# Kernel tuning notes

Hardware: AMD Instinct MI355X
Metric: run time of the kernel (lower is better)

The kernel has to match this reference:

```python
import jax, jax.numpy as jnp
import numpy as np
import math

B, SQ, SK, D = 32, 2048, 2048, 128


def setup_inputs() -> dict:
    key = jax.random.key(0)
    kq, kk, kv = jax.random.split(key, 3)
    queries = jax.random.normal(kq, (B, SQ, D), dtype=jnp.float32)
    keys = jax.random.normal(kk, (B, SK, D), dtype=jnp.float32)
    values = jax.random.normal(kv, (B, SK, D), dtype=jnp.float32)
    # causal mask: True = masked (future positions), broadcast over batch
    causal = jnp.triu(jnp.ones((SQ, SK), dtype=bool), k=1)
    mask = jnp.broadcast_to(causal, (B, SQ, SK))
    return {"queries": queries, "keys": keys, "values": values, "mask": mask}


def reference(queries, keys, values, mask):
    d = queries.shape[-1]
    scale = 1.0 / math.sqrt(d)
    # [B, Sq, Sk] score matrix (the module materializes this explicitly)
    scores = jnp.einsum("bqd,bkd->bqk", queries, keys) * scale
    scores = jnp.where(mask, -jnp.inf, scores)
    attn = jax.nn.softmax(scores, axis=-1)
    # dropout p=0.0 -> identity (eval parity)
    return jnp.einsum("bqk,bkd->bqd", attn, values)
```

## Files before the change

### kernel.cpp

```cpp
#include <hip/hip_runtime.h>
#include <hip/hip_bf16.h>

#define NB   32
#define SQL  2048
#define DH   128
#define QBLK 128
#define KBLK 64
#define NKT  (SQL / KBLK)
#define TILEB 16384

typedef __attribute__((ext_vector_type(4)))  float f32x4;
typedef __attribute__((ext_vector_type(16))) float f32x16;
typedef __attribute__((ext_vector_type(8)))  short s16x8;
typedef __attribute__((ext_vector_type(4)))  unsigned int u32x4;

__device__ __forceinline__ unsigned int cvtpk_bf16(float lo, float hi) {
  unsigned int r;
  asm("v_cvt_pk_bf16_f32 %0, %1, %2" : "=v"(r) : "v"(lo), "v"(hi));
  return r;
}
#define PLSWAP(x, y) asm volatile("v_permlane32_swap_b32 %0, %1" : "+v"(x), "+v"(y))

__device__ __forceinline__ unsigned int pk2(float lo, float hi) {
  unsigned short a = __builtin_bit_cast(unsigned short, __float2bfloat16(lo));
  unsigned short b = __builtin_bit_cast(unsigned short, __float2bfloat16(hi));
  return (unsigned int)a | ((unsigned int)b << 16);
}

#define AS1(p) ((const __attribute__((address_space(1))) void*)(p))
#define AS3(p) ((__attribute__((address_space(3))) void*)(p))

__global__ __launch_bounds__(256)
void prep_kv(const float* __restrict__ Kg, const float* __restrict__ Vg,
             char* __restrict__ wsK, char* __restrict__ wsV) {
  const int blk = blockIdx.x;
  const int b   = blk >> 5;
  const int kt  = blk & 31;
  const int tid = threadIdx.x;
  const float* Ksrc = Kg + ((size_t)b * SQL + (size_t)kt * KBLK) * DH;
  const float* Vsrc = Vg + ((size_t)b * SQL + (size_t)kt * KBLK) * DH;
  char* Kdst = wsK + (size_t)blk * TILEB;
  char* Vdst = wsV + (size_t)blk * TILEB;

  {
    const int q16 = tid & 15;
    const int r0  = tid >> 4;
    #pragma unroll
    for (int it = 0; it < 4; ++it) {
      const int r = r0 + 16 * it;
      const float* src = Ksrc + (size_t)r * DH + 8 * q16;
      f32x4 a = *(const f32x4*)(src);
      f32x4 d = *(const f32x4*)(src + 4);
      u32x4 w;
      w[0] = pk2(a[0], a[1]); w[1] = pk2(a[2], a[3]);
      w[2] = pk2(d[0], d[1]); w[3] = pk2(d[2], d[3]);
      *(u32x4*)(Kdst + ((r * 256 + 16 * q16) ^ ((r & 7) << 4))) = w;
    }
  }
  {
    const int kq = tid & 15;
    const int dq = tid >> 4;
    #pragma unroll
    for (int it = 0; it < 2; ++it) {
      const int d0 = 4 * dq + 64 * it;
      f32x4 rv[4];
      #pragma unroll
      for (int j = 0; j < 4; ++j)
        rv[j] = *(const f32x4*)(Vsrc + (size_t)(4 * kq + j) * DH + d0);
      #pragma unroll
      for (int j2 = 0; j2 < 4; ++j2) {
        const int dd = d0 + j2;
        uint2 w = make_uint2(pk2(rv[0][j2], rv[1][j2]), pk2(rv[2][j2], rv[3][j2]));
        *(uint2*)(Vdst + ((dd * 128 + 8 * kq) ^ ((dd & 7) << 4))) = w;
      }
    }
  }
}

__global__ __launch_bounds__(256, 2)
void attn_fwd(const float* __restrict__ Qg, const char* __restrict__ wsK,
              const char* __restrict__ wsV, float* __restrict__ Og) {
  __shared__ __align__(16) char smem[65536];

  const int tid  = threadIdx.x;
  const int wid  = tid >> 6;
  const int lane = tid & 63;
  const int hi   = lane >> 5;
  const int c    = lane & 31;

  const int i    = blockIdx.x;
  const int half = i >> 8;
  const int j    = i & 255;
  const int b    = j & 31;
  const int q3   = j >> 5;
  const int qt   = half ? (15 - q3) : q3;
  const int qb   = qt * QBLK;
  const int nt   = 2 * qt + 2;

  const float* Qb = Qg + (size_t)b * SQL * DH;
  float* Ob = Og + (size_t)b * SQL * DH;
  const char* Ktiles = wsK + (size_t)b * NKT * TILEB;
  const char* Vtiles = wsV + (size_t)b * NKT * TILEB;

  const float qscale = 0.08838834764831845f * 1.4426950408889634f;

  s16x8 qf[8];
  {
    const float* qr = Qb + (size_t)(qb + 32*wid + c) * DH + 8*hi;
    #pragma unroll
    for (int ds = 0; ds < 8; ++ds) {
      f32x4 a = *(const f32x4*)(qr + 16*ds);
      f32x4 d = *(const f32x4*)(qr + 16*ds + 4);
      u32x4 w;
      w[0] = pk2(a[0]*qscale, a[1]*qscale);
      w[1] = pk2(a[2]*qscale, a[3]*qscale);
      w[2] = pk2(d[0]*qscale, d[1]*qscale);
      w[3] = pk2(d[2]*qscale, d[3]*qscale);
      qf[ds] = __builtin_bit_cast(s16x8, w);
    }
  }

  f32x16 oacc[4];
  #pragma unroll
  for (int nb = 0; nb < 4; ++nb) oacc[nb] = (f32x16){0.f};
  float m_run = -1e30f, l_run = 0.f;

  const int qglob = qb + 32*wid + c;
  const int qhiw  = qb + 32*wid + 31;
  const int qlow  = qb + 32*wid;

  auto STAGE = [&](int t) {
    const char* ks = Ktiles + (size_t)t * TILEB + tid * 16;
    const char* vs = Vtiles + (size_t)t * TILEB + tid * 16;
    char* kl = smem + (t & 1) * 16384 + wid * 1024;
    char* vl = smem + 32768 + (t & 1) * 16384 + wid * 1024;
    #pragma unroll
    for (int jj = 0; jj < 4; ++jj) {
      __builtin_amdgcn_global_load_lds(AS1(ks + jj * 4096), AS3(kl + jj * 4096), 16, 0, 0);
      __builtin_amdgcn_global_load_lds(AS1(vs + jj * 4096), AS3(vl + jj * 4096), 16, 0, 0);
    }
  };

  STAGE(0);

  for (int t = 0; t < nt; ++t) {
    asm volatile("s_waitcnt vmcnt(0)" ::: "memory");
    __builtin_amdgcn_s_barrier();
    __builtin_amdgcn_sched_barrier(0);
    if (t + 1 < nt) STAGE(t + 1);

    const int kb = t * KBLK;
    const char* Kl = smem + (t & 1) * 16384;
    const char* Vl = smem + 32768 + (t & 1) * 16384;

    if (kb <= qhiw) {
      f32x16 sacc[2];
      sacc[0] = (f32x16){0.f};
      sacc[1] = (f32x16){0.f};
      __builtin_amdgcn_s_setprio(1);
      #pragma unroll
      for (int ds = 0; ds < 8; ++ds) {
        #pragma unroll
        for (int mb = 0; mb < 2; ++mb) {
          const int row = 32*mb + c;
          s16x8 kf = *(const s16x8*)(Kl + ((row*256 + 32*ds + 16*hi) ^ ((c & 7) << 4)));
          sacc[mb] = __builtin_amdgcn_mfma_f32_32x32x16_bf16(kf, qf[ds], sacc[mb], 0, 0, 0);
        }
      }
      __builtin_amdgcn_s_setprio(0);

      s16x8 vka[4], vkb[4];
      #pragma unroll
      for (int nb = 0; nb < 4; ++nb) {
        const int row = 32*nb + c;
        vka[nb] = *(const s16x8*)(Vl + ((row*128 +  0 + 16*hi) ^ ((c & 7) << 4)));
        vkb[nb] = *(const s16x8*)(Vl + ((row*128 + 32 + 16*hi) ^ ((c & 7) << 4)));
      }

      if (kb + KBLK - 1 > qlow) {
        #pragma unroll
        for (int mb = 0; mb < 2; ++mb)
          #pragma unroll
          for (int r = 0; r < 16; ++r) {
            const int kk = kb + 32*mb + (r & 3) + 8*(r >> 2) + 4*hi;
            if (kk > qglob) sacc[mb][r] = -1e30f;
          }
      }

      float mx[8];
      #pragma unroll
      for (int e = 0; e < 8; ++e)
        mx[e] = fmaxf(fmaxf(sacc[0][e], sacc[0][e+8]), fmaxf(sacc[1][e], sacc[1][e+8]));
      mx[0] = fmaxf(mx[0], mx[4]); mx[1] = fmaxf(mx[1], mx[5]);
      mx[2] = fmaxf(mx[2], mx[6]); mx[3] = fmaxf(mx[3], mx[7]);
      const float tmax = fmaxf(fmaxf(mx[0], mx[1]), fmaxf(mx[2], mx[3]));

      if (!__all(tmax <= m_run + 8.0f)) {
        float tfull = fmaxf(tmax, __shfl_xor(tmax, 32));
        const float mnew  = fmaxf(m_run, tfull);
        const float alpha = exp2f(m_run - mnew);
        #pragma unroll
        for (int r = 0; r < 16; ++r) {
          float av = __shfl(alpha, (r & 3) + 8*(r >> 2) + 4*hi);
          #pragma unroll
          for (int nb = 0; nb < 4; ++nb) oacc[nb][r] *= av;
        }
        l_run *= alpha;
        m_run = mnew;
      }

      float lsa = 0.f, lsb = 0.f;
      unsigned int u0[8], u1[8];
      #pragma unroll
      for (int w = 0; w < 8; ++w) {
        float p0 = exp2f(sacc[0][2*w]     - m_run);
        float p1 = exp2f(sacc[0][2*w + 1] - m_run);
        lsa += p0 + p1;
        u0[w] = cvtpk_bf16(p0, p1);
      }
      #pragma unroll
      for (int w = 0; w < 8; ++w) {
        float p0 = exp2f(sacc[1][2*w]     - m_run);
        float p1 = exp2f(sacc[1][2*w + 1] - m_run);
        lsb += p0 + p1;
        u1[w] = cvtpk_bf16(p0, p1);
      }
      l_run += lsa + lsb;

      s16x8 vkc[4], vkd[4];
      #pragma unroll
      for (int nb = 0; nb < 4; ++nb) {
        const int row = 32*nb + c;
        vkc[nb] = *(const s16x8*)(Vl + ((row*128 + 64 + 16*hi) ^ ((c & 7) << 4)));
        vkd[nb] = *(const s16x8*)(Vl + ((row*128 + 96 + 16*hi) ^ ((c & 7) << 4)));
      }

      PLSWAP(u0[0], u0[2]); PLSWAP(u0[1], u0[3]);
      PLSWAP(u0[4], u0[6]); PLSWAP(u0[5], u0[7]);
      PLSWAP(u1[0], u1[2]); PLSWAP(u1[1], u1[3]);
      PLSWAP(u1[4], u1[6]); PLSWAP(u1[5], u1[7]);
      s16x8 pa[4];
      { u32x4 w = {u0[0], u0[1], u0[2], u0[3]}; pa[0] = __builtin_bit_cast(s16x8, w); }
      { u32x4 w = {u0[4], u0[5], u0[6], u0[7]}; pa[1] = __builtin_bit_cast(s16x8, w); }
      { u32x4 w = {u1[0], u1[1], u1[2], u1[3]}; pa[2] = __builtin_bit_cast(s16x8, w); }
      { u32x4 w = {u1[4], u1[5], u1[6], u1[7]}; pa[3] = __builtin_bit_cast(s16x8, w); }

      __builtin_amdgcn_s_setprio(1);
      #pragma unroll
      for (int nb = 0; nb < 4; ++nb)
        oacc[nb] = __builtin_amdgcn_mfma_f32_32x32x16_bf16(pa[0], vka[nb], oacc[nb], 0, 0, 0);
      #pragma unroll
      for (int nb = 0; nb < 4; ++nb)
        oacc[nb] = __builtin_amdgcn_mfma_f32_32x32x16_bf16(pa[1], vkb[nb], oacc[nb], 0, 0, 0);
      #pragma unroll
      for (int nb = 0; nb < 4; ++nb)
        oacc[nb] = __builtin_amdgcn_mfma_f32_32x32x16_bf16(pa[2], vkc[nb], oacc[nb], 0, 0, 0);
      #pragma unroll
      for (int nb = 0; nb < 4; ++nb)
        oacc[nb] = __builtin_amdgcn_mfma_f32_32x32x16_bf16(pa[3], vkd[nb], oacc[nb], 0, 0, 0);
      __builtin_amdgcn_s_setprio(0);
    }
  }

  const float l_tot = l_run + __shfl_xor(l_run, 32);
  const float linv  = 1.0f / l_tot;
  float* Orow = Ob + (size_t)(qb + 32*wid) * DH;
  #pragma unroll
  for (int r = 0; r < 16; ++r) {
    const int q = (r & 3) + 8*(r >> 2) + 4*hi;
    float lv = __shfl(linv, q);
    #pragma unroll
    for (int nb = 0; nb < 4; ++nb)
      Orow[(size_t)q * DH + 32*nb + c] = oacc[nb][r] * lv;
  }
}

extern "C" void kernel_launch(void* const* d_in, const int* in_sizes, int n_in,
                              void* d_out, int out_size, void* d_ws, size_t ws_size,
                              hipStream_t stream) {
  const float* Q = (const float*)d_in[0];
  const float* K = (const float*)d_in[1];
  const float* V = (const float*)d_in[2];
  float* O = (float*)d_out;
  char* wsK = (char*)d_ws;
  char* wsV = (char*)d_ws + (size_t)NB * NKT * TILEB;

  prep_kv<<<dim3(NB * NKT), dim3(256), 0, stream>>>(K, V, wsK, wsV);
  attn_fwd<<<dim3(NB * (SQL / QBLK)), dim3(256), 0, stream>>>(Q, wsK, wsV, O);
}
```

Baseline: 84.05 us.

## Fuse K/V bf16 preprocessing into attention kernel with per-tile ready flags

Removes the separate prep_kv launch. Each attention block now converts two K/V tiles itself, writes them to the workspace and publishes a release flag. When a block stages a tile, it checks that tile's flag: if the tile is ready it uses async global-to-LDS loads, otherwise it converts the fp32 K/V directly into LDS. This saves one kernel launch and the serialization between the two kernels. In exchange it adds a memset, per-tile atomic flag reads, extra barriers and redundant conversion work when tiles are not ready yet.

```diff
diff --git a/kernel.cpp b/kernel.cpp
--- a/kernel.cpp
+++ b/kernel.cpp
@@ -30,18 +30,14 @@
 #define AS1(p) ((const __attribute__((address_space(1))) void*)(p))
 #define AS3(p) ((__attribute__((address_space(3))) void*)(p))
 
-__global__ __launch_bounds__(256)
-void prep_kv(const float* __restrict__ Kg, const float* __restrict__ Vg,
-             char* __restrict__ wsK, char* __restrict__ wsV) {
-  const int blk = blockIdx.x;
-  const int b   = blk >> 5;
-  const int kt  = blk & 31;
-  const int tid = threadIdx.x;
+__device__ __forceinline__ void prep_tile(const float* __restrict__ Kg,
+                                          const float* __restrict__ Vg,
+                                          char* __restrict__ wsK, char* __restrict__ wsV,
+                                          int b, int kt, int tid) {
   const float* Ksrc = Kg + ((size_t)b * SQL + (size_t)kt * KBLK) * DH;
   const float* Vsrc = Vg + ((size_t)b * SQL + (size_t)kt * KBLK) * DH;
-  char* Kdst = wsK + (size_t)blk * TILEB;
-  char* Vdst = wsV + (size_t)blk * TILEB;
-
+  char* Kdst = wsK + ((size_t)b * NKT + kt) * TILEB;
+  char* Vdst = wsV + ((size_t)b * NKT + kt) * TILEB;
   {
     const int q16 = tid & 15;
     const int r0  = tid >> 4;
@@ -78,9 +74,12 @@
 }
 
 __global__ __launch_bounds__(256, 2)
-void attn_fwd(const float* __restrict__ Qg, const char* __restrict__ wsK,
-              const char* __restrict__ wsV, float* __restrict__ Og) {
+void attn_fused(const float* __restrict__ Qg, const float* __restrict__ Kg,
+                const float* __restrict__ Vg, char* __restrict__ wsK,
+                char* __restrict__ wsV, unsigned* __restrict__ flags,
+                float* __restrict__ Og) {
   __shared__ __align__(16) char smem[65536];
+  __shared__ int rdy[2];
 
   const int tid  = threadIdx.x;
   const int wid  = tid >> 6;
@@ -101,6 +100,14 @@
   float* Ob = Og + (size_t)b * SQL * DH;
   const char* Ktiles = wsK + (size_t)b * NKT * TILEB;
   const char* Vtiles = wsV + (size_t)b * NKT * TILEB;
+
+  prep_tile(Kg, Vg, wsK, wsV, b, qt, tid);
+  prep_tile(Kg, Vg, wsK, wsV, b, 16 + qt, tid);
+  __syncthreads();
+  if (tid == 0) {
+    __hip_atomic_store(&flags[b * NKT + qt], 1u, __ATOMIC_RELEASE, __HIP_MEMORY_SCOPE_AGENT);
+    __hip_atomic_store(&flags[b * NKT + 16 + qt], 1u, __ATOMIC_RELEASE, __HIP_MEMORY_SCOPE_AGENT);
+  }
 
   const float qscale = 0.08838834764831845f * 1.4426950408889634f;
 
@@ -129,25 +136,69 @@
   const int qhiw  = qb + 32*wid + 31;
   const int qlow  = qb + 32*wid;
 
-  auto STAGE = [&](int t) {
-    const char* ks = Ktiles + (size_t)t * TILEB + tid * 16;
-    const char* vs = Vtiles + (size_t)t * TILEB + tid * 16;
-    char* kl = smem + (t & 1) * 16384 + wid * 1024;
-    char* vl = smem + 32768 + (t & 1) * 16384 + wid * 1024;
-    #pragma unroll
-    for (int jj = 0; jj < 4; ++jj) {
-      __builtin_amdgcn_global_load_lds(AS1(ks + jj * 4096), AS3(kl + jj * 4096), 16, 0, 0);
-      __builtin_amdgcn_global_load_lds(AS1(vs + jj * 4096), AS3(vl + jj * 4096), 16, 0, 0);
-    }
+  auto FLAGREAD = [&](int t) -> int {
+    return (int)__hip_atomic_load(&flags[b * NKT + t], __ATOMIC_ACQUIRE,
+                                  __HIP_MEMORY_SCOPE_AGENT);
   };
 
-  STAGE(0);
+  auto STAGE = [&](int t, bool ready) {
+    char* kl = smem + (t & 1) * 16384;
+    char* vl = smem + 32768 + (t & 1) * 16384;
+    if (ready) {
+      const char* ks = Ktiles + (size_t)t * TILEB + tid * 16;
+      const char* vs = Vtiles + (size_t)t * TILEB + tid * 16;
+      char* klw = kl + wid * 1024;
+      char* vlw = vl + wid * 1024;
+      #pragma unroll
+      for (int jj = 0; jj < 4; ++jj) {
+        __builtin_amdgcn_global_load_lds(AS1(ks + jj * 4096), AS3(klw + jj * 4096), 16, 0, 0);
+        __builtin_amdgcn_global_load_lds(AS1(vs + jj * 4096), AS3(vlw + jj * 4096), 16, 0, 0);
+      }
+    } else {
+      const float* Ksrc = Kg + ((size_t)b * SQL + (size_t)t * KBLK) * DH;
+      const float* Vsrc = Vg + ((size_t)b * SQL + (size_t)t * KBLK) * DH;
+      const int q16 = tid & 15;
+      const int r0  = tid >> 4;
+      #pragma unroll
+      for (int it = 0; it < 4; ++it) {
+        const int r = r0 + 16 * it;
+        const float* src = Ksrc + (size_t)r * DH + 8 * q16;
+        f32x4 a = *(const f32x4*)(src);
+        f32x4 d = *(const f32x4*)(src + 4);
+        u32x4 w;
+        w[0] = pk2(a[0], a[1]); w[1] = pk2(a[2], a[3]);
+        w[2] = pk2(d[0], d[1]); w[3] = pk2(d[2], d[3]);
+        *(u32x4*)(kl + ((r * 256 + 16 * q16) ^ ((r & 7) << 4))) = w;
+      }
+      const int kq = tid & 15;
+      const int dq = tid >> 4;
+      #pragma unroll
+      for (int it = 0; it < 2; ++it) {
+        const int d0 = 4 * dq + 64 * it;
+        f32x4 rv[4];
+        #pragma unroll
+        for (int jv = 0; jv < 4; ++jv)
+          rv[jv] = *(const f32x4*)(Vsrc + (size_t)(4 * kq + jv) * DH + d0);
+        #pragma unroll
+        for (int j2 = 0; j2 < 4; ++j2) {
+          const int dd = d0 + j2;
+          uint2 w = make_uint2(pk2(rv[0][j2], rv[1][j2]), pk2(rv[2][j2], rv[3][j2]));
+          *(uint2*)(vl + ((dd * 128 + 8 * kq) ^ ((dd & 7) << 4))) = w;
+        }
+      }
+    }
+  };
+
+  if (tid == 0) rdy[0] = FLAGREAD(0);
+  __syncthreads();
+  STAGE(0, rdy[0] == 1);
 
   for (int t = 0; t < nt; ++t) {
-    asm volatile("s_waitcnt vmcnt(0)" ::: "memory");
+    if (t + 1 < nt && tid == 0) rdy[(t + 1) & 1] = FLAGREAD(t + 1);
+    asm volatile("s_waitcnt vmcnt(0) lgkmcnt(0)" ::: "memory");
     __builtin_amdgcn_s_barrier();
     __builtin_amdgcn_sched_barrier(0);
-    if (t + 1 < nt) STAGE(t + 1);
+    if (t + 1 < nt) STAGE(t + 1, rdy[(t + 1) & 1] == 1);
 
     const int kb = t * KBLK;
     const char* Kl = smem + (t & 1) * 16384;
@@ -284,7 +335,8 @@
   float* O = (float*)d_out;
   char* wsK = (char*)d_ws;
   char* wsV = (char*)d_ws + (size_t)NB * NKT * TILEB;
-
-  prep_kv<<<dim3(NB * NKT), dim3(256), 0, stream>>>(K, V, wsK, wsV);
-  attn_fwd<<<dim3(NB * (SQL / QBLK)), dim3(256), 0, stream>>>(Q, wsK, wsV, O);
-}
+  unsigned* flags = (unsigned*)((char*)d_ws + (size_t)2 * NB * NKT * TILEB);
+
+  hipMemsetAsync(flags, 0, NB * NKT * sizeof(unsigned), stream);
+  attn_fused<<<dim3(512), dim3(256), 0, stream>>>(Q, K, V, wsK, wsV, flags, O);
+}
```

Result: slower. 143.1 us (+70.3%).

## Split long causal query tiles across two blocks and merge partial softmax results

Applied to the files above, without the earlier changes.

Query tiles 8-15, which carry the most key tiles under the causal mask, are each split into two blocks covering halves of the key range. Each half writes bf16 partial outputs plus running max and sum to workspace, and a new merge kernel combines them with the log-sum-exp rescale. A constant slot table orders the blocks longest-first to balance load across the grid. The cost is an extra kernel launch, extra global traffic for the partial outputs, and some precision loss from storing the partials in bf16.

```diff
diff --git a/kernel.cpp b/kernel.cpp
--- a/kernel.cpp
+++ b/kernel.cpp
@@ -26,9 +26,18 @@
   unsigned short b = __builtin_bit_cast(unsigned short, __float2bfloat16(hi));
   return (unsigned int)a | ((unsigned int)b << 16);
 }
+__device__ __forceinline__ unsigned short f2bf(float f) {
+  return __builtin_bit_cast(unsigned short, __float2bfloat16(f));
+}
+__device__ __forceinline__ float bf2f(unsigned short u) {
+  return __builtin_bit_cast(float, (unsigned int)u << 16);
+}
 
 #define AS1(p) ((const __attribute__((address_space(1))) void*)(p))
 #define AS3(p) ((__attribute__((address_space(3))) void*)(p))
+
+__constant__ signed char SLOT_QT[24]   = {15,15,7,14,14,6,13,13,12,12,5,11,11,10,10,4,9,9,8,8,3,2,1,0};
+__constant__ signed char SLOT_PART[24] = { 0, 1,2, 0, 1,2, 0, 1, 0, 1,2, 0, 1, 0, 1,2,0,1,0,1,2,2,2,2};
 
 __global__ __launch_bounds__(256)
 void prep_kv(const float* __restrict__ Kg, const float* __restrict__ Vg,
@@ -78,8 +87,9 @@
 }
 
 __global__ __launch_bounds__(256, 2)
-void attn_fwd(const float* __restrict__ Qg, const char* __restrict__ wsK,
-              const char* __restrict__ wsV, float* __restrict__ Og) {
+void attn_split(const float* __restrict__ Qg, const char* __restrict__ wsK,
+                const char* __restrict__ wsV, float* __restrict__ Og,
+                unsigned short* __restrict__ wsOp, float2* __restrict__ wsMl) {
   __shared__ __align__(16) char smem[65536];
 
   const int tid  = threadIdx.x;
@@ -89,13 +99,14 @@
   const int c    = lane & 31;
 
   const int i    = blockIdx.x;
-  const int half = i >> 8;
-  const int j    = i & 255;
-  const int b    = j & 31;
-  const int q3   = j >> 5;
-  const int qt   = half ? (15 - q3) : q3;
+  const int b    = i & 31;
+  const int slot = i >> 5;
+  const int qt   = SLOT_QT[slot];
+  const int part = SLOT_PART[slot];
   const int qb   = qt * QBLK;
   const int nt   = 2 * qt + 2;
+  const int t0   = (part == 1) ? (qt + 1) : 0;
+  const int t1   = (part == 0) ? (qt + 1) : nt;
 
   const float* Qb = Qg + (size_t)b * SQL * DH;
   float* Ob = Og + (size_t)b * SQL * DH;
@@ -141,13 +152,13 @@
     }
   };
 
-  STAGE(0);
-
-  for (int t = 0; t < nt; ++t) {
+  STAGE(t0);
+
+  for (int t = t0; t < t1; ++t) {
     asm volatile("s_waitcnt vmcnt(0)" ::: "memory");
     __builtin_amdgcn_s_barrier();
     __builtin_amdgcn_sched_barrier(0);
-    if (t + 1 < nt) STAGE(t + 1);
+    if (t + 1 < t1) STAGE(t + 1);
 
     const int kb = t * KBLK;
     const char* Kl = smem + (t & 1) * 16384;
@@ -263,15 +274,68 @@
   }
 
   const float l_tot = l_run + __shfl_xor(l_run, 32);
-  const float linv  = 1.0f / l_tot;
-  float* Orow = Ob + (size_t)(qb + 32*wid) * DH;
+  if (part == 2) {
+    const float linv = 1.0f / l_tot;
+    float* Orow = Ob + (size_t)(qb + 32*wid) * DH;
+    #pragma unroll
+    for (int r = 0; r < 16; ++r) {
+      const int q = (r & 3) + 8*(r >> 2) + 4*hi;
+      float lv = __shfl(linv, q);
+      #pragma unroll
+      for (int nb = 0; nb < 4; ++nb)
+        Orow[(size_t)q * DH + 32*nb + c] = oacc[nb][r] * lv;
+    }
+  } else {
+    const int qi = qt - 8;
+    const size_t tile = ((size_t)part * NB + b) * 8 + qi;
+    if (hi == 0)
+      wsMl[tile * QBLK + 32*wid + c] = make_float2(m_run, l_tot);
+    unsigned short* op = wsOp + (tile * QBLK + 32*wid) * DH;
+    #pragma unroll
+    for (int r = 0; r < 16; ++r) {
+      const int q = (r & 3) + 8*(r >> 2) + 4*hi;
+      #pragma unroll
+      for (int nb = 0; nb < 4; ++nb)
+        op[(size_t)q * DH + 32*nb + c] = f2bf(oacc[nb][r]);
+    }
+  }
+}
+
+__global__ __launch_bounds__(256)
+void merge_split(const unsigned short* __restrict__ wsOp,
+                 const float2* __restrict__ wsMl, float* __restrict__ Og) {
+  const int blk = blockIdx.x;
+  const int b   = blk >> 3;
+  const int qi  = blk & 7;
+  const int qt  = 8 + qi;
+  const int row   = threadIdx.x >> 1;
+  const int chalf = threadIdx.x & 1;
+
+  const size_t tile0 = ((size_t)0 * NB + b) * 8 + qi;
+  const size_t tile1 = ((size_t)1 * NB + b) * 8 + qi;
+  const float2 ml0 = wsMl[tile0 * QBLK + row];
+  const float2 ml1 = wsMl[tile1 * QBLK + row];
+  const float m  = fmaxf(ml0.x, ml1.x);
+  float w0 = exp2f(ml0.x - m);
+  float w1 = exp2f(ml1.x - m);
+  const float inv = 1.0f / (ml0.y * w0 + ml1.y * w1);
+  w0 *= inv; w1 *= inv;
+
+  const unsigned short* p0 = wsOp + (tile0 * QBLK + row) * DH + chalf * 64;
+  const unsigned short* p1 = wsOp + (tile1 * QBLK + row) * DH + chalf * 64;
+  float* out = Og + ((size_t)b * SQL + (size_t)qt * QBLK + row) * DH + chalf * 64;
   #pragma unroll
-  for (int r = 0; r < 16; ++r) {
-    const int q = (r & 3) + 8*(r >> 2) + 4*hi;
-    float lv = __shfl(linv, q);
-    #pragma unroll
-    for (int nb = 0; nb < 4; ++nb)
-      Orow[(size_t)q * DH + 32*nb + c] = oacc[nb][r] * lv;
+  for (int g = 0; g < 8; ++g) {
+    s16x8 a = *(const s16x8*)(p0 + 8 * g);
+    s16x8 d = *(const s16x8*)(p1 + 8 * g);
+    f32x4 o0, o1;
+    #pragma unroll
+    for (int e = 0; e < 4; ++e) {
+      o0[e] = bf2f((unsigned short)a[e])     * w0 + bf2f((unsigned short)d[e])     * w1;
+      o1[e] = bf2f((unsigned short)a[e + 4]) * w0 + bf2f((unsigned short)d[e + 4]) * w1;
+    }
+    *(f32x4*)(out + 8 * g)     = o0;
+    *(f32x4*)(out + 8 * g + 4) = o1;
   }
 }
 
@@ -283,8 +347,11 @@
   const float* V = (const float*)d_in[2];
   float* O = (float*)d_out;
   char* wsK = (char*)d_ws;
-  char* wsV = (char*)d_ws + (size_t)NB * NKT * TILEB;
+  char* wsV = wsK + (size_t)NB * NKT * TILEB;
+  unsigned short* wsOp = (unsigned short*)(wsV + (size_t)NB * NKT * TILEB);
+  float2* wsMl = (float2*)((char*)wsOp + (size_t)2 * NB * 8 * QBLK * DH * sizeof(unsigned short));
 
   prep_kv<<<dim3(NB * NKT), dim3(256), 0, stream>>>(K, V, wsK, wsV);
-  attn_fwd<<<dim3(NB * (SQL / QBLK)), dim3(256), 0, stream>>>(Q, wsK, wsV, O);
-}
+  attn_split<<<dim3(NB * 24), dim3(256), 0, stream>>>(Q, wsK, wsV, O, wsOp, wsMl);
+  merge_split<<<dim3(NB * 8), dim3(256), 0, stream>>>(wsOp, wsMl, O);
+}
```

After: 90.98 us. 1.08x slower.
